# Performance work log

Hardware: AMD Instinct MI355X
Metric: run time of the kernel (lower is better)

Reference implementation:

```python
import jax, jax.numpy as jnp
import numpy as np

N = 500_000
D = 128           # input_dim
A = 128           # attention_dim
O = 1             # output_dim (broadcasts over input_dim)
B = 256           # number of repertoires (segments)


def setup_inputs() -> dict:
    key = jax.random.key(0)
    k1, k2, k3, k4 = jax.random.split(key, 4)
    x = jax.random.normal(k1, (N, D), dtype=jnp.float32)
    batch_index = jnp.sort(jax.random.randint(k2, (N,), 0, B, dtype=jnp.int32))
    # attention MLP params: Linear(D->A), Tanh, Linear(A->O)
    W1 = jax.random.normal(k3, (D, A), dtype=jnp.float32) * (1.0 / np.sqrt(D))
    b1 = jnp.zeros((A,), dtype=jnp.float32)
    W2 = jax.random.normal(k4, (A, O), dtype=jnp.float32) * (1.0 / np.sqrt(A))
    b2 = jnp.zeros((O,), dtype=jnp.float32)
    return {"x": x, "batch_index": batch_index, "W1": W1, "b1": b1, "W2": W2, "b2": b2}


def reference(x, batch_index, W1, b1, W2, b2):
    # per-instance attention score: Linear -> Tanh -> Linear
    h = jnp.tanh(x @ W1 + b1)          # [N, A]
    scores = h @ W2 + b2               # [N, O]
    # segment softmax over instances within each repertoire
    seg_max = jax.ops.segment_max(scores, batch_index, num_segments=B)   # [B, O]
    e = jnp.exp(scores - seg_max[batch_index])                           # [N, O]
    denom = jax.ops.segment_sum(e, batch_index, num_segments=B)          # [B, O]
    w = e / denom[batch_index]                                           # [N, O]
    # weighted sum of instance features per repertoire (O=1 broadcasts over D)
    out = jax.ops.segment_sum(w * x, batch_index, num_segments=B)        # [B, D]
    return out
```

## Files before the change

### kernel.cpp

```cpp
#include <hip/hip_runtime.h>
#include <math.h>

#define D_DIM 128
#define A_DIM 128
#define SPLIT 4
#define NTHREADS 256
#define NWAVES 4
#define PSTRIDE 132

typedef _Float16 f16x8 __attribute__((ext_vector_type(8)));
typedef __attribute__((ext_vector_type(4))) float f32x4;

__device__ __forceinline__ float fast_tanh(float v) {
    float e = __expf(2.0f * v);
    return 1.0f - 2.0f * __builtin_amdgcn_rcpf(e + 1.0f);
}

__device__ __forceinline__ int lower_bound_i32(const int* __restrict__ arr, int n, int val) {
    int lo = 0, hi = n;
    while (lo < hi) {
        int mid = (lo + hi) >> 1;
        if (arr[mid] < val) lo = mid + 1; else hi = mid;
    }
    return lo;
}

extern "C" __global__ void __launch_bounds__(256)
seg_bounds_kernel(const int* __restrict__ bidx, int N, int B,
                  int* __restrict__ seg_start)
{
    const int i = blockIdx.x * 256 + threadIdx.x;
    if (i <= B) seg_start[i] = lower_bound_i32(bidx, N, i);
}

extern "C" __global__ void __launch_bounds__(NTHREADS)
fused_partial_kernel(const float* __restrict__ x,
                     const int* __restrict__ seg_start,
                     const float* __restrict__ W1,
                     const float* __restrict__ b1,
                     const float* __restrict__ W2,
                     float* __restrict__ part,
                     int N)
{
    __shared__ _Float16 w1s[A_DIM * D_DIM];
    __shared__ float sB1[A_DIM];
    __shared__ float sW2[A_DIM];
    __shared__ float s_sc[NWAVES * 16];
    __shared__ float o_red[NWAVES * 4 * 32];
    __shared__ float s_d[NWAVES];

    const int tid = threadIdx.x;
    const int b   = blockIdx.x >> 2;
    const int q   = blockIdx.x & (SPLIT - 1);

    if (tid < A_DIM) { sB1[tid] = b1[tid]; sW2[tid] = W2[tid]; }

    for (int item = tid; item < A_DIM * 16; item += NTHREADS) {
        const int c = item & (A_DIM - 1);
        const int chunk = item >> 7;
        f16x8 vh;
        #pragma unroll
        for (int j = 0; j < 8; ++j)
            vh[j] = (_Float16)W1[(chunk * 8 + j) * A_DIM + c];
        const int addr = c * 256 + ((chunk ^ (c & 15)) << 4);
        *reinterpret_cast<f16x8*>(reinterpret_cast<char*>(w1s) + addr) = vh;
    }
    __syncthreads();

    const int lo  = seg_start[b];
    const int len = seg_start[b + 1] - lo;
    const int qper = (((len + SPLIT - 1) / SPLIT) + 63) & ~63;
    const int q0   = q * qper;
    const int qlen = min(qper, len - q0);
    const int ntl  = (qlen + 63) >> 6;

    const int lane = tid & 63;
    const int wv   = tid >> 6;
    const int lc   = lane & 15;
    const int lg   = lane >> 4;
    const int rowoff = q0 + wv * 16 + lc;

    float den = 0.0f;
    float o_part[32];
    #pragma unroll
    for (int v = 0; v < 32; ++v) o_part[v] = 0.0f;

    float4 buf[8];
    if (ntl > 0) {
        const int gi = min(lo + rowoff, N - 1);
        const float4* xr = reinterpret_cast<const float4*>(x + (size_t)gi * D_DIM);
        #pragma unroll
        for (int ks = 0; ks < 4; ++ks) {
            buf[2*ks]   = xr[ks*8 + lg*2];
            buf[2*ks+1] = xr[ks*8 + lg*2 + 1];
        }
    }

    for (int t = 0; t < ntl; ++t) {
        f16x8 ah[4], al[4];
        #pragma unroll
        for (int ks = 0; ks < 4; ++ks) {
            const float4 v0 = buf[2*ks];
            const float4 v1 = buf[2*ks+1];
            _Float16 h;
            h = (_Float16)v0.x; ah[ks][0] = h; al[ks][0] = (_Float16)(v0.x - (float)h);
            h = (_Float16)v0.y; ah[ks][1] = h; al[ks][1] = (_Float16)(v0.y - (float)h);
            h = (_Float16)v0.z; ah[ks][2] = h; al[ks][2] = (_Float16)(v0.z - (float)h);
            h = (_Float16)v0.w; ah[ks][3] = h; al[ks][3] = (_Float16)(v0.w - (float)h);
            h = (_Float16)v1.x; ah[ks][4] = h; al[ks][4] = (_Float16)(v1.x - (float)h);
            h = (_Float16)v1.y; ah[ks][5] = h; al[ks][5] = (_Float16)(v1.y - (float)h);
            h = (_Float16)v1.z; ah[ks][6] = h; al[ks][6] = (_Float16)(v1.z - (float)h);
            h = (_Float16)v1.w; ah[ks][7] = h; al[ks][7] = (_Float16)(v1.w - (float)h);
        }

        if (t + 1 < ntl) {
            const int gi = min(lo + rowoff + (t + 1) * 64, N - 1);
            const float4* xr = reinterpret_cast<const float4*>(x + (size_t)gi * D_DIM);
            #pragma unroll
            for (int ks = 0; ks < 4; ++ks) {
                buf[2*ks]   = xr[ks*8 + lg*2];
                buf[2*ks+1] = xr[ks*8 + lg*2 + 1];
            }
        }

        __builtin_amdgcn_s_setprio(1);
        float part0 = 0.f, part1 = 0.f, part2 = 0.f, part3 = 0.f;
        #pragma unroll
        for (int tt = 0; tt < 8; ++tt) {
            f32x4 acc = {0.f, 0.f, 0.f, 0.f};
            const int c = tt * 16 + lc;
            const char* base = reinterpret_cast<const char*>(w1s) + c * 256;
            #pragma unroll
            for (int ks = 0; ks < 4; ++ks) {
                const int chunk = ks * 4 + lg;
                f16x8 bh = *reinterpret_cast<const f16x8*>(
                    base + ((chunk ^ (c & 15)) << 4));
                acc = __builtin_amdgcn_mfma_f32_16x16x32_f16(ah[ks], bh, acc, 0, 0, 0);
                acc = __builtin_amdgcn_mfma_f32_16x16x32_f16(al[ks], bh, acc, 0, 0, 0);
            }
            const float b1v = sB1[c], w2v = sW2[c];
            part0 += fast_tanh(acc[0] + b1v) * w2v;
            part1 += fast_tanh(acc[1] + b1v) * w2v;
            part2 += fast_tanh(acc[2] + b1v) * w2v;
            part3 += fast_tanh(acc[3] + b1v) * w2v;
        }
        __builtin_amdgcn_s_setprio(0);

        #pragma unroll
        for (int mk = 8; mk >= 1; mk >>= 1) {
            part0 += __shfl_xor(part0, mk);
            part1 += __shfl_xor(part1, mk);
            part2 += __shfl_xor(part2, mk);
            part3 += __shfl_xor(part3, mk);
        }
        if (lc == 0) {
            float* sl = &s_sc[wv * 16 + lg * 4];
            sl[0] = part0; sl[1] = part1; sl[2] = part2; sl[3] = part3;
        }
        const float my_s = s_sc[wv * 16 + lc];
        const float w = (rowoff + t * 64 < len) ? __expf(my_s) : 0.0f;
        den += w;

        #pragma unroll
        for (int ks = 0; ks < 4; ++ks) {
            #pragma unroll
            for (int j = 0; j < 8; ++j) {
                const int v = ks * 8 + j;
                o_part[v] = fmaf(w, (float)ah[ks][j] + (float)al[ks][j], o_part[v]);
            }
        }
    }

    #pragma unroll
    for (int v = 0; v < 32; ++v) {
        #pragma unroll
        for (int mk = 8; mk >= 1; mk >>= 1)
            o_part[v] += __shfl_xor(o_part[v], mk);
    }
    #pragma unroll
    for (int mk = 8; mk >= 1; mk >>= 1) den += __shfl_xor(den, mk);

    if (lc == 0) {
        #pragma unroll
        for (int v = 0; v < 32; ++v)
            o_red[(wv * 4 + lg) * 32 + v] = o_part[v];
        if (lg == 0) s_d[wv] = den;
    }
    __syncthreads();

    float* pb = part + (size_t)blockIdx.x * PSTRIDE;
    if (tid < 128) {
        const int lg2 = tid >> 5, v = tid & 31;
        float val = 0.0f;
        #pragma unroll
        for (int w2 = 0; w2 < NWAVES; ++w2) val += o_red[(w2 * 4 + lg2) * 32 + v];
        const int d = (v >> 3) * 32 + lg2 * 8 + (v & 7);
        pb[d] = val;
        if (tid == 0)
            pb[128] = s_d[0] + s_d[1] + s_d[2] + s_d[3];
    }
}

extern "C" __global__ void __launch_bounds__(128)
combine_kernel(const float* __restrict__ part, float* __restrict__ out)
{
    const int b = blockIdx.x, d = threadIdx.x;
    const float* pb = part + (size_t)b * SPLIT * PSTRIDE;

    float den = 0.0f, val = 0.0f;
    #pragma unroll
    for (int q = 0; q < SPLIT; ++q) {
        den += pb[q * PSTRIDE + 128];
        val += pb[q * PSTRIDE + d];
    }
    out[b * D_DIM + d] = (den > 0.0f) ? val / den : 0.0f;
}

extern "C" void kernel_launch(void* const* d_in, const int* in_sizes, int n_in,
                              void* d_out, int out_size, void* d_ws, size_t ws_size,
                              hipStream_t stream)
{
    const float* x    = (const float*)d_in[0];
    const int*   bidx = (const int*)d_in[1];
    const float* W1   = (const float*)d_in[2];
    const float* b1   = (const float*)d_in[3];
    const float* W2   = (const float*)d_in[4];

    const int N = in_sizes[1];
    const int B = out_size / D_DIM;

    char* ws = (char*)d_ws;
    int*   seg_start = (int*)ws;
    float* part      = (float*)(ws + 4096);

    seg_bounds_kernel<<<(B + 256) / 256, 256, 0, stream>>>(bidx, N, B, seg_start);
    fused_partial_kernel<<<B * SPLIT, NTHREADS, 0, stream>>>(
        x, seg_start, W1, b1, W2, part, N);
    combine_kernel<<<B, 128, 0, stream>>>(part, (float*)d_out);
}
```

Before: 89.05 us.

## Drop fp16 low-part split MFMA and double-buffer x loads in registers

Removes the hi/lo fp16 split of x so each k-step issues one MFMA instead of two, and converts with packed cvt_pkrtz. The weighted feature sum now uses the original fp32 values held in registers. A manual ping-pong of two register buffers replaces the single buffer so the next tile's load does not overwrite data still needed. The cost is lower score precision (round-toward-zero fp16 x against fp16 W1) and higher register pressure from the second buffer.

```diff
diff --git a/kernel.cpp b/kernel.cpp
--- a/kernel.cpp
+++ b/kernel.cpp
@@ -9,6 +9,7 @@
 #define PSTRIDE 132
 
 typedef _Float16 f16x8 __attribute__((ext_vector_type(8)));
+typedef __fp16   fp16x2 __attribute__((ext_vector_type(2)));
 typedef __attribute__((ext_vector_type(4))) float f32x4;
 
 __device__ __forceinline__ float fast_tanh(float v) {
@@ -85,91 +86,96 @@
     #pragma unroll
     for (int v = 0; v < 32; ++v) o_part[v] = 0.0f;
 
-    float4 buf[8];
+    float4 bufA[8], bufB[8];
     if (ntl > 0) {
         const int gi = min(lo + rowoff, N - 1);
         const float4* xr = reinterpret_cast<const float4*>(x + (size_t)gi * D_DIM);
         #pragma unroll
         for (int ks = 0; ks < 4; ++ks) {
-            buf[2*ks]   = xr[ks*8 + lg*2];
-            buf[2*ks+1] = xr[ks*8 + lg*2 + 1];
+            bufA[2*ks]   = xr[ks*8 + lg*2];
+            bufA[2*ks+1] = xr[ks*8 + lg*2 + 1];
         }
     }
 
-    for (int t = 0; t < ntl; ++t) {
-        f16x8 ah[4], al[4];
-        #pragma unroll
-        for (int ks = 0; ks < 4; ++ks) {
-            const float4 v0 = buf[2*ks];
-            const float4 v1 = buf[2*ks+1];
-            _Float16 h;
-            h = (_Float16)v0.x; ah[ks][0] = h; al[ks][0] = (_Float16)(v0.x - (float)h);
-            h = (_Float16)v0.y; ah[ks][1] = h; al[ks][1] = (_Float16)(v0.y - (float)h);
-            h = (_Float16)v0.z; ah[ks][2] = h; al[ks][2] = (_Float16)(v0.z - (float)h);
-            h = (_Float16)v0.w; ah[ks][3] = h; al[ks][3] = (_Float16)(v0.w - (float)h);
-            h = (_Float16)v1.x; ah[ks][4] = h; al[ks][4] = (_Float16)(v1.x - (float)h);
-            h = (_Float16)v1.y; ah[ks][5] = h; al[ks][5] = (_Float16)(v1.y - (float)h);
-            h = (_Float16)v1.z; ah[ks][6] = h; al[ks][6] = (_Float16)(v1.z - (float)h);
-            h = (_Float16)v1.w; ah[ks][7] = h; al[ks][7] = (_Float16)(v1.w - (float)h);
+#define PROC_TILE(CUR, NXT, T)                                                 \
+    {                                                                          \
+                     \
+        f16x8 ah[4];                                                           \
+        _Pragma("unroll")                                                      \
+        for (int ks = 0; ks < 4; ++ks) {                                       \
+            union { f16x8 v; fp16x2 h[4]; } u;                                 \
+            u.h[0] = __builtin_amdgcn_cvt_pkrtz(CUR[2*ks].x,   CUR[2*ks].y);   \
+            u.h[1] = __builtin_amdgcn_cvt_pkrtz(CUR[2*ks].z,   CUR[2*ks].w);   \
+            u.h[2] = __builtin_amdgcn_cvt_pkrtz(CUR[2*ks+1].x, CUR[2*ks+1].y); \
+            u.h[3] = __builtin_amdgcn_cvt_pkrtz(CUR[2*ks+1].z, CUR[2*ks+1].w); \
+            ah[ks] = u.v;                                                      \
+        }                                                                      \
+        if ((T) + 1 < ntl) {                                                   \
+            const int gi = min(lo + rowoff + ((T) + 1) * 64, N - 1);           \
+            const float4* xr =                                                 \
+                reinterpret_cast<const float4*>(x + (size_t)gi * D_DIM);       \
+            _Pragma("unroll")                                                  \
+            for (int ks = 0; ks < 4; ++ks) {                                   \
+                NXT[2*ks]   = xr[ks*8 + lg*2];                                 \
+                NXT[2*ks+1] = xr[ks*8 + lg*2 + 1];                             \
+            }                                                                  \
+        }                                                                      \
+        __builtin_amdgcn_s_setprio(1);                                         \
+        float part0 = 0.f, part1 = 0.f, part2 = 0.f, part3 = 0.f;              \
+        _Pragma("unroll")                                                      \
+        for (int tt = 0; tt < 8; ++tt) {                                       \
+            f32x4 acc = {0.f, 0.f, 0.f, 0.f};                                  \
+            const int c = tt * 16 + lc;                                        \
+            const char* base = reinterpret_cast<const char*>(w1s) + c * 256;   \
+            _Pragma("unroll")                                                  \
+            for (int ks = 0; ks < 4; ++ks) {                                   \
+                const int chunk = ks * 4 + lg;                                 \
+                f16x8 bh = *reinterpret_cast<const f16x8*>(                    \
+                    base + ((chunk ^ (c & 15)) << 4));                         \
+                acc = __builtin_amdgcn_mfma_f32_16x16x32_f16(ah[ks], bh, acc,  \
+                                                             0, 0, 0);         \
+            }                                                                  \
+            const float b1v = sB1[c], w2v = sW2[c];                            \
+            part0 += fast_tanh(acc[0] + b1v) * w2v;                            \
+            part1 += fast_tanh(acc[1] + b1v) * w2v;                            \
+            part2 += fast_tanh(acc[2] + b1v) * w2v;                            \
+            part3 += fast_tanh(acc[3] + b1v) * w2v;                            \
+        }                                                                      \
+        __builtin_amdgcn_s_setprio(0);                                         \
+        _Pragma("unroll")                                                      \
+        for (int mk = 8; mk >= 1; mk >>= 1) {                                  \
+            part0 += __shfl_xor(part0, mk);                                    \
+            part1 += __shfl_xor(part1, mk);                                    \
+            part2 += __shfl_xor(part2, mk);                                    \
+            part3 += __shfl_xor(part3, mk);                                    \
+        }                                                                      \
+        if (lc == 0) {                                                         \
+            float* sl = &s_sc[wv * 16 + lg * 4];                               \
+            sl[0] = part0; sl[1] = part1; sl[2] = part2; sl[3] = part3;        \
+        }                                                                      \
+        const float my_s = s_sc[wv * 16 + lc];                                 \
+        const float w = (rowoff + (T) * 64 < len) ? __expf(my_s) : 0.0f;       \
+        den += w;                                                              \
+        _Pragma("unroll")                                                      \
+        for (int ks = 0; ks < 4; ++ks) {                                       \
+            o_part[ks*8+0] = fmaf(w, CUR[2*ks].x,   o_part[ks*8+0]);           \
+            o_part[ks*8+1] = fmaf(w, CUR[2*ks].y,   o_part[ks*8+1]);           \
+            o_part[ks*8+2] = fmaf(w, CUR[2*ks].z,   o_part[ks*8+2]);           \
+            o_part[ks*8+3] = fmaf(w, CUR[2*ks].w,   o_part[ks*8+3]);           \
+            o_part[ks*8+4] = fmaf(w, CUR[2*ks+1].x, o_part[ks*8+4]);           \
+            o_part[ks*8+5] = fmaf(w, CUR[2*ks+1].y, o_part[ks*8+5]);           \
+            o_part[ks*8+6] = fmaf(w, CUR[2*ks+1].z, o_part[ks*8+6]);           \
+            o_part[ks*8+7] = fmaf(w, CUR[2*ks+1].w, o_part[ks*8+7]);           \
+        }                                                                      \
+    }
+
+    for (int t = 0; t < ntl; t += 2) {
+        PROC_TILE(bufA, bufB, t);
+        if (t + 1 < ntl) {
+            PROC_TILE(bufB, bufA, t + 1);
         }
-
-        if (t + 1 < ntl) {
-            const int gi = min(lo + rowoff + (t + 1) * 64, N - 1);
-            const float4* xr = reinterpret_cast<const float4*>(x + (size_t)gi * D_DIM);
-            #pragma unroll
-            for (int ks = 0; ks < 4; ++ks) {
-                buf[2*ks]   = xr[ks*8 + lg*2];
-                buf[2*ks+1] = xr[ks*8 + lg*2 + 1];
-            }
-        }
-
-        __builtin_amdgcn_s_setprio(1);
-        float part0 = 0.f, part1 = 0.f, part2 = 0.f, part3 = 0.f;
-        #pragma unroll
-        for (int tt = 0; tt < 8; ++tt) {
-            f32x4 acc = {0.f, 0.f, 0.f, 0.f};
-            const int c = tt * 16 + lc;
-            const char* base = reinterpret_cast<const char*>(w1s) + c * 256;
-            #pragma unroll
-            for (int ks = 0; ks < 4; ++ks) {
-                const int chunk = ks * 4 + lg;
-                f16x8 bh = *reinterpret_cast<const f16x8*>(
-                    base + ((chunk ^ (c & 15)) << 4));
-                acc = __builtin_amdgcn_mfma_f32_16x16x32_f16(ah[ks], bh, acc, 0, 0, 0);
-                acc = __builtin_amdgcn_mfma_f32_16x16x32_f16(al[ks], bh, acc, 0, 0, 0);
-            }
-            const float b1v = sB1[c], w2v = sW2[c];
-            part0 += fast_tanh(acc[0] + b1v) * w2v;
-            part1 += fast_tanh(acc[1] + b1v) * w2v;
-            part2 += fast_tanh(acc[2] + b1v) * w2v;
-            part3 += fast_tanh(acc[3] + b1v) * w2v;
-        }
-        __builtin_amdgcn_s_setprio(0);
-
-        #pragma unroll
-        for (int mk = 8; mk >= 1; mk >>= 1) {
-            part0 += __shfl_xor(part0, mk);
-            part1 += __shfl_xor(part1, mk);
-            part2 += __shfl_xor(part2, mk);
-            part3 += __shfl_xor(part3, mk);
-        }
-        if (lc == 0) {
-            float* sl = &s_sc[wv * 16 + lg * 4];
-            sl[0] = part0; sl[1] = part1; sl[2] = part2; sl[3] = part3;
-        }
-        const float my_s = s_sc[wv * 16 + lc];
-        const float w = (rowoff + t * 64 < len) ? __expf(my_s) : 0.0f;
-        den += w;
-
-        #pragma unroll
-        for (int ks = 0; ks < 4; ++ks) {
-            #pragma unroll
-            for (int j = 0; j < 8; ++j) {
-                const int v = ks * 8 + j;
-                o_part[v] = fmaf(w, (float)ah[ks][j] + (float)al[ks][j], o_part[v]);
-            }
-        }
-    }
+    }
+#undef PROC_TILE
 
     #pragma unroll
     for (int v = 0; v < 32; ++v) {
```

Measured after the change: 102.8 us. 15.4% more time.
